# Kernel optimization log

Measured on AMD Instinct MI355X. Metric: run time of the kernel, lower is better.

The kernel has to match this reference:

```python
import jax, jax.numpy as jnp
import numpy as np

B, F, D = 1024, 39, 16
HIDDEN = [128, 128, 128]


def _cin(x, Ws, bs):
    # x: (B, F0, D) stacked field embeddings
    F0 = x.shape[1]
    h = x  # hidden_nn_layers[-1], shape (B, Fk, D)
    outs = []
    n = len(Ws)
    for i, (W, b) in enumerate(zip(Ws, bs)):
        L = W.shape[-1]
        Fk = h.shape[1]
        Wr = W.reshape(F0, Fk, L)  # conv1d kernel [1, F0*Fk, L] -> (F0, Fk, L)
        # per-embedding-dim field outer product: (B, F0, Fk, D)
        z = jnp.einsum('bfd,bgd->bfgd', x, h)
        # pointwise conv over D + bias + relu -> (B, L, D)
        cur = jax.nn.relu(jnp.einsum('bfgd,fgl->bld', z, Wr) + b[None, :, None])
        if i != n - 1:
            h = cur[:, : L // 2]          # next_hidden
            direct = cur[:, L // 2 :]     # direct_connect
        else:
            direct = cur
        outs.append(direct)
    # concat over field axis, sum over embedding dim -> (B, sum_direct)
    return jnp.concatenate(outs, axis=1).sum(-1)


def setup_inputs() -> dict:
    key = jax.random.key(0)
    ks = jax.random.split(key, 8)
    x = jax.random.normal(ks[0], (B, F, D), dtype=jnp.float32)
    field_nums = [F]
    Ws, bs = [], []
    for i, L in enumerate(HIDDEN):
        fan_in = field_nums[0] * field_nums[-1]
        lim = np.sqrt(6.0 / fan_in)  # he_uniform
        Ws.append(jax.random.uniform(ks[1 + i], (fan_in, L), jnp.float32, -lim, lim))
        bs.append(jnp.zeros((L,), jnp.float32))
        field_nums.append(L // 2)
    return {"x": x, "W0": Ws[0], "W1": Ws[1], "W2": Ws[2],
            "b0": bs[0], "b1": bs[1], "b2": bs[2]}


def reference(x, W0, W1, W2, b0, b1, b2):
    return _cin(x, [W0, W1, W2], [b0, b1, b2])
```

## Files before the change

kernel.cpp:

```cpp
#include <hip/hip_runtime.h>


#define NF     39
#define LCH    128
#define NLAYER 3
#define NFT    (NLAYER * NF)
#define BPB    2
#define SL     (BPB * 16)
#define MT     (SL / 16)

typedef __bf16        bf16x8 __attribute__((ext_vector_type(8)));
typedef unsigned int  uint4v __attribute__((ext_vector_type(4)));
typedef float         f32x4  __attribute__((ext_vector_type(4)));

__device__ __forceinline__ unsigned short f2bf_rne(float f) {
    unsigned u = __float_as_uint(f);
    u += 0x7fffu + ((u >> 16) & 1u);
    return (unsigned short)(u >> 16);
}

__global__ void cin_prep(const float* __restrict__ W0,
                         const float* __restrict__ W1,
                         const float* __restrict__ W2,
                         unsigned short* __restrict__ wt)
{
    const int t = blockIdx.x * blockDim.x + threadIdx.x;
    if (t >= NFT * 1024) return;
    const int n  = t & 127;
    const int q  = (t >> 7) & 3;
    const int ks = (t >> 9) & 1;
    const int tl = t >> 10;
    const int l  = tl / NF;
    const int f  = tl - l * NF;
    const float* W = (l == 0) ? W0 : (l == 1) ? W1 : W2;

    unsigned short v[8];
    #pragma unroll
    for (int j = 0; j < 8; ++j) {
        const int g = ks * 32 + q * 8 + j;
        float w = 0.0f;
        if (l == 0) { if (g < NF) w = W[(f * NF + g) * LCH + n]; }
        else        { w = W[(f * 64 + g) * LCH + n]; }
        v[j] = f2bf_rne(w);
    }
    uint4v pv;
    #pragma unroll
    for (int i = 0; i < 4; ++i)
        pv[i] = (unsigned)v[2 * i] | ((unsigned)v[2 * i + 1] << 16);
    ((uint4v*)wt)[t] = pv;
}

__global__ __launch_bounds__(512, 4) void cin_mfma(
    const float* __restrict__ x,
    const unsigned short* __restrict__ wt,
    const float* __restrict__ b0p,
    const float* __restrict__ b1p,
    const float* __restrict__ b2p,
    float* __restrict__ out)
{
    __shared__ __align__(16) unsigned short hfrag[8 * SL * 8];
    __shared__ float xf32[NF * SL];
    __shared__ float biasl[NLAYER * LCH];

    const int tid  = threadIdx.x;
    const int lane = tid & 63;
    const int w    = tid >> 6;
    const int q    = lane >> 4;
    const int c    = lane & 15;
    const int nc   = w * 16 + c;
    const int bb   = blockIdx.x * BPB;

    {
        f32x4 z4 = {0.f, 0.f, 0.f, 0.f};
        if (tid < (8 * SL * 8) / 8) ((f32x4*)hfrag)[tid] = z4;
    }
    for (int t = tid; t < NLAYER * LCH; t += 512)
        biasl[t] = (t < 128) ? b0p[t] : (t < 256) ? b1p[t - 128] : b2p[t - 256];
    __syncthreads();

    for (int i = tid; i < BPB * NF * 16; i += 512) {
        const float v = x[bb * (NF * 16) + i];
        const int lb = i / (NF * 16);
        const int r  = i - lb * (NF * 16);
        const int f  = r >> 4;
        const int d  = r & 15;
        const int sl = lb * 16 + d;
        xf32[f * SL + sl] = v;
        hfrag[((f >> 3) * SL + sl) * 8 + (f & 7)] = f2bf_rne(v);
    }

    const unsigned short* wq = wt + (q * 128 + nc) * 8;

    bf16x8 c0 = *(const bf16x8*)(wq);
    bf16x8 c1 = *(const bf16x8*)(wq + 4096);
    bf16x8 m0 = *(const bf16x8*)(wq + 8192);
    bf16x8 m1 = *(const bf16x8*)(wq + 8192 + 4096);
    bf16x8 n0 = *(const bf16x8*)(wq + 16384);
    bf16x8 n1 = *(const bf16x8*)(wq + 16384 + 4096);

    __syncthreads();

    #pragma unroll 1
    for (int l = 0; l < NLAYER; ++l) {
        bf16x8 a[2][MT];
        #pragma unroll
        for (int ks = 0; ks < 2; ++ks)
            #pragma unroll
            for (int mt = 0; mt < MT; ++mt)
                a[ks][mt] = *(const bf16x8*)&hfrag[((ks * 4 + q) * SL + mt * 16 + c) * 8];

        f32x4 cur[MT];
        #pragma unroll
        for (int mt = 0; mt < MT; ++mt) cur[mt] = f32x4{0.f, 0.f, 0.f, 0.f};
        const f32x4 z = {0.f, 0.f, 0.f, 0.f};

        #pragma unroll 3
        for (int f = 0; f < NF; ++f) {
            const bf16x8 bv0 = c0;
            const bf16x8 bv1 = c1;

            #pragma unroll
            for (int mt = 0; mt < MT; ++mt) {
                f32x4 sv = __builtin_amdgcn_mfma_f32_16x16x32_bf16(a[0][mt], bv0, z,  0, 0, 0);
                sv       = __builtin_amdgcn_mfma_f32_16x16x32_bf16(a[1][mt], bv1, sv, 0, 0, 0);
                const f32x4 xr = *(const f32x4*)&xf32[f * SL + mt * 16 + q * 4];
                #pragma unroll
                for (int r = 0; r < 4; ++r)
                    cur[mt][r] = fmaf(xr[r], sv[r], cur[mt][r]);
            }

            c0 = m0; c1 = m1;
            m0 = n0; m1 = n1;
            int pf = l * NF + f + 3; if (pf > NFT - 1) pf = NFT - 1;
            const unsigned short* p = wq + (size_t)pf * 8192;
            n0 = *(const bf16x8*)p;
            n1 = *(const bf16x8*)(p + 4096);
        }

        const float bias = biasl[l * LCH + nc];
        float v[MT][4];
        #pragma unroll
        for (int mt = 0; mt < MT; ++mt)
            #pragma unroll
            for (int r = 0; r < 4; ++r)
                v[mt][r] = fmaxf(cur[mt][r] + bias, 0.f);

        if (l < 2 && w < 4) {
            #pragma unroll
            for (int mt = 0; mt < MT; ++mt)
                #pragma unroll
                for (int r = 0; r < 4; ++r)
                    hfrag[((nc >> 3) * SL + mt * 16 + q * 4 + r) * 8 + (nc & 7)] =
                        f2bf_rne(v[mt][r]);
        } else {
            const int outcol = (l == 0) ? nc - 64 : (l == 1) ? nc : 128 + nc;
            #pragma unroll
            for (int mt = 0; mt < MT; ++mt) {
                float sacc = v[mt][0] + v[mt][1] + v[mt][2] + v[mt][3];
                sacc += __shfl_xor(sacc, 16, 64);
                sacc += __shfl_xor(sacc, 32, 64);
                if (lane < 16) out[(bb + mt) * 256 + outcol] = sacc;
            }
        }
        if (l < 2) __syncthreads();
    }
}

extern "C" void kernel_launch(void* const* d_in, const int* in_sizes, int n_in,
                              void* d_out, int out_size, void* d_ws, size_t ws_size,
                              hipStream_t stream) {
    const float* x  = (const float*)d_in[0];
    const float* W0 = (const float*)d_in[1];
    const float* W1 = (const float*)d_in[2];
    const float* W2 = (const float*)d_in[3];
    const float* b0 = (const float*)d_in[4];
    const float* b1 = (const float*)d_in[5];
    const float* b2 = (const float*)d_in[6];
    float* out = (float*)d_out;
    unsigned short* wt = (unsigned short*)d_ws;

    const int prep_threads = NFT * 1024;
    cin_prep<<<(prep_threads + 255) / 256, 256, 0, stream>>>(W0, W1, W2, wt);
    cin_mfma<<<1024 / BPB, 512, 0, stream>>>(x, wt, b0, b1, b2, out);
}
```

Baseline: 107.5 us.

## Stage weight tiles in LDS via async double-buffered loads and share across waves

The change doubles the batch rows per block and doubles threads to 1024, with two wave groups along M. Each wave group shares the same weight tiles. Weights are no longer streamed from global memory into registers per wave; they are copied into a double-buffered LDS staging area with global_load_lds, three fields per phase. This halves redundant global weight traffic per batch element and overlaps the next phase's load with the current MFMAs. In exchange it adds a block-wide barrier every three fields and uses about 96KB of LDS, which limits occupancy.

```diff
diff --git a/kernel.cpp b/kernel.cpp
--- a/kernel.cpp
+++ b/kernel.cpp
@@ -1,13 +1,16 @@
 #include <hip/hip_runtime.h>
 
 
-#define NF     39
-#define LCH    128
-#define NLAYER 3
-#define NFT    (NLAYER * NF)
-#define BPB    2
-#define SL     (BPB * 16)
-#define MT     (SL / 16)
+#define NF      39
+#define LCH     128
+#define NLAYER  3
+#define NFT     (NLAYER * NF)
+#define BPB     4
+#define SL      (BPB * 16)
+#define NTHR    1024
+#define TILE_SH 8192
+#define PH_T    3
+#define BUF_SH  (PH_T * TILE_SH)
 
 typedef __bf16        bf16x8 __attribute__((ext_vector_type(8)));
 typedef unsigned int  uint4v __attribute__((ext_vector_type(4)));
@@ -50,7 +53,7 @@
     ((uint4v*)wt)[t] = pv;
 }
 
-__global__ __launch_bounds__(512, 4) void cin_mfma(
+__global__ __launch_bounds__(NTHR, 4) void cin_mfma(
     const float* __restrict__ x,
     const unsigned short* __restrict__ wt,
     const float* __restrict__ b0p,
@@ -58,6 +61,7 @@
     const float* __restrict__ b2p,
     float* __restrict__ out)
 {
+    __shared__ __align__(16) unsigned short Bbuf[2 * BUF_SH];
     __shared__ __align__(16) unsigned short hfrag[8 * SL * 8];
     __shared__ float xf32[NF * SL];
     __shared__ float biasl[NLAYER * LCH];
@@ -65,20 +69,22 @@
     const int tid  = threadIdx.x;
     const int lane = tid & 63;
     const int w    = tid >> 6;
+    const int wn   = w & 7;
+    const int wm   = w >> 3;
     const int q    = lane >> 4;
     const int c    = lane & 15;
-    const int nc   = w * 16 + c;
+    const int nc   = wn * 16 + c;
     const int bb   = blockIdx.x * BPB;
 
-    {
+    if (tid < 512) {
         f32x4 z4 = {0.f, 0.f, 0.f, 0.f};
-        if (tid < (8 * SL * 8) / 8) ((f32x4*)hfrag)[tid] = z4;
-    }
-    for (int t = tid; t < NLAYER * LCH; t += 512)
-        biasl[t] = (t < 128) ? b0p[t] : (t < 256) ? b1p[t - 128] : b2p[t - 256];
+        ((f32x4*)hfrag)[tid] = z4;
+    }
+    if (tid < NLAYER * LCH)
+        biasl[tid] = (tid < 128) ? b0p[tid] : (tid < 256) ? b1p[tid - 128] : b2p[tid - 256];
     __syncthreads();
 
-    for (int i = tid; i < BPB * NF * 16; i += 512) {
+    for (int i = tid; i < BPB * NF * 16; i += NTHR) {
         const float v = x[bb * (NF * 16) + i];
         const int lb = i / (NF * 16);
         const int r  = i - lb * (NF * 16);
@@ -89,77 +95,103 @@
         hfrag[((f >> 3) * SL + sl) * 8 + (f & 7)] = f2bf_rne(v);
     }
 
-    const unsigned short* wq = wt + (q * 128 + nc) * 8;
-
-    bf16x8 c0 = *(const bf16x8*)(wq);
-    bf16x8 c1 = *(const bf16x8*)(wq + 4096);
-    bf16x8 m0 = *(const bf16x8*)(wq + 8192);
-    bf16x8 m1 = *(const bf16x8*)(wq + 8192 + 4096);
-    bf16x8 n0 = *(const bf16x8*)(wq + 16384);
-    bf16x8 n1 = *(const bf16x8*)(wq + 16384 + 4096);
-
+    {
+        const unsigned short* src = wt + w * 512 + lane * 8;
+        unsigned short* dst = Bbuf + w * 512;
+        #pragma unroll
+        for (int k = 0; k < PH_T; ++k)
+            __builtin_amdgcn_global_load_lds((const void*)(src + k * TILE_SH),
+                                             (void*)(dst + k * TILE_SH), 16, 0, 0);
+    }
     __syncthreads();
+
+    const unsigned short* bq = Bbuf + (q * 128 + nc) * 8;
+
+    int cb = 0;
+    int tl = 0;
 
     #pragma unroll 1
     for (int l = 0; l < NLAYER; ++l) {
-        bf16x8 a[2][MT];
+        bf16x8 a[2][2];
         #pragma unroll
         for (int ks = 0; ks < 2; ++ks)
             #pragma unroll
-            for (int mt = 0; mt < MT; ++mt)
-                a[ks][mt] = *(const bf16x8*)&hfrag[((ks * 4 + q) * SL + mt * 16 + c) * 8];
-
-        f32x4 cur[MT];
+            for (int mtl = 0; mtl < 2; ++mtl)
+                a[ks][mtl] = *(const bf16x8*)
+                    &hfrag[((ks * 4 + q) * SL + (wm * 2 + mtl) * 16 + c) * 8];
+
+        f32x4 cur0 = {0.f, 0.f, 0.f, 0.f};
+        f32x4 cur1 = {0.f, 0.f, 0.f, 0.f};
+        const f32x4 z = {0.f, 0.f, 0.f, 0.f};
+
+        #pragma unroll 1
+        for (int ph = 0; ph < NF / PH_T; ++ph) {
+            const int nb = tl + PH_T;
+            if (nb < NFT) {
+                const unsigned short* src = wt + (size_t)nb * TILE_SH + w * 512 + lane * 8;
+                unsigned short* dst = &Bbuf[(cb ^ 1) * BUF_SH + w * 512];
+                #pragma unroll
+                for (int k = 0; k < PH_T; ++k)
+                    __builtin_amdgcn_global_load_lds((const void*)(src + k * TILE_SH),
+                                                     (void*)(dst + k * TILE_SH), 16, 0, 0);
+            }
+
+            const unsigned short* rb = bq + cb * BUF_SH;
+            const bf16x8 B00 = *(const bf16x8*)(rb);
+            const bf16x8 B01 = *(const bf16x8*)(rb + 4096);
+            const bf16x8 B10 = *(const bf16x8*)(rb + TILE_SH);
+            const bf16x8 B11 = *(const bf16x8*)(rb + TILE_SH + 4096);
+            const bf16x8 B20 = *(const bf16x8*)(rb + 2 * TILE_SH);
+            const bf16x8 B21 = *(const bf16x8*)(rb + 2 * TILE_SH + 4096);
+
+            const int f0 = ph * PH_T;
+            #define CIN_ITER(BV0, BV1, FI)                                              \
+            {                                                                           \
+                f32x4 sv0 = __builtin_amdgcn_mfma_f32_16x16x32_bf16(a[0][0], BV0, z, 0, 0, 0); \
+                sv0 = __builtin_amdgcn_mfma_f32_16x16x32_bf16(a[1][0], BV1, sv0, 0, 0, 0);     \
+                f32x4 sv1 = __builtin_amdgcn_mfma_f32_16x16x32_bf16(a[0][1], BV0, z, 0, 0, 0); \
+                sv1 = __builtin_amdgcn_mfma_f32_16x16x32_bf16(a[1][1], BV1, sv1, 0, 0, 0);     \
+                const f32x4 xr0 = *(const f32x4*)&xf32[(FI) * SL + (wm * 2 + 0) * 16 + q * 4]; \
+                const f32x4 xr1 = *(const f32x4*)&xf32[(FI) * SL + (wm * 2 + 1) * 16 + q * 4]; \
+                _Pragma("unroll")                                                       \
+                for (int r = 0; r < 4; ++r) {                                           \
+                    cur0[r] = fmaf(xr0[r], sv0[r], cur0[r]);                            \
+                    cur1[r] = fmaf(xr1[r], sv1[r], cur1[r]);                            \
+                }                                                                       \
+            }
+            CIN_ITER(B00, B01, f0 + 0)
+            CIN_ITER(B10, B11, f0 + 1)
+            CIN_ITER(B20, B21, f0 + 2)
+            #undef CIN_ITER
+
+            __syncthreads();
+            cb ^= 1;
+            tl += PH_T;
+        }
+
+        const float bias = biasl[l * LCH + nc];
+        float v[2][4];
         #pragma unroll
-        for (int mt = 0; mt < MT; ++mt) cur[mt] = f32x4{0.f, 0.f, 0.f, 0.f};
-        const f32x4 z = {0.f, 0.f, 0.f, 0.f};
-
-        #pragma unroll 3
-        for (int f = 0; f < NF; ++f) {
-            const bf16x8 bv0 = c0;
-            const bf16x8 bv1 = c1;
-
+        for (int r = 0; r < 4; ++r) {
+            v[0][r] = fmaxf(cur0[r] + bias, 0.f);
+            v[1][r] = fmaxf(cur1[r] + bias, 0.f);
+        }
+
+        if (l < 2 && wn < 4) {
             #pragma unroll
-            for (int mt = 0; mt < MT; ++mt) {
-                f32x4 sv = __builtin_amdgcn_mfma_f32_16x16x32_bf16(a[0][mt], bv0, z,  0, 0, 0);
-                sv       = __builtin_amdgcn_mfma_f32_16x16x32_bf16(a[1][mt], bv1, sv, 0, 0, 0);
-                const f32x4 xr = *(const f32x4*)&xf32[f * SL + mt * 16 + q * 4];
+            for (int mtl = 0; mtl < 2; ++mtl)
                 #pragma unroll
                 for (int r = 0; r < 4; ++r)
-                    cur[mt][r] = fmaf(xr[r], sv[r], cur[mt][r]);
-            }
-
-            c0 = m0; c1 = m1;
-            m0 = n0; m1 = n1;
-            int pf = l * NF + f + 3; if (pf > NFT - 1) pf = NFT - 1;
-            const unsigned short* p = wq + (size_t)pf * 8192;
-            n0 = *(const bf16x8*)p;
-            n1 = *(const bf16x8*)(p + 4096);
-        }
-
-        const float bias = biasl[l * LCH + nc];
-        float v[MT][4];
-        #pragma unroll
-        for (int mt = 0; mt < MT; ++mt)
-            #pragma unroll
-            for (int r = 0; r < 4; ++r)
-                v[mt][r] = fmaxf(cur[mt][r] + bias, 0.f);
-
-        if (l < 2 && w < 4) {
-            #pragma unroll
-            for (int mt = 0; mt < MT; ++mt)
-                #pragma unroll
-                for (int r = 0; r < 4; ++r)
-                    hfrag[((nc >> 3) * SL + mt * 16 + q * 4 + r) * 8 + (nc & 7)] =
-                        f2bf_rne(v[mt][r]);
+                    hfrag[((nc >> 3) * SL + (wm * 2 + mtl) * 16 + q * 4 + r) * 8 + (nc & 7)] =
+                        f2bf_rne(v[mtl][r]);
         } else {
             const int outcol = (l == 0) ? nc - 64 : (l == 1) ? nc : 128 + nc;
             #pragma unroll
-            for (int mt = 0; mt < MT; ++mt) {
-                float sacc = v[mt][0] + v[mt][1] + v[mt][2] + v[mt][3];
+            for (int mtl = 0; mtl < 2; ++mtl) {
+                float sacc = v[mtl][0] + v[mtl][1] + v[mtl][2] + v[mtl][3];
                 sacc += __shfl_xor(sacc, 16, 64);
                 sacc += __shfl_xor(sacc, 32, 64);
-                if (lane < 16) out[(bb + mt) * 256 + outcol] = sacc;
+                if (lane < 16) out[(bb + wm * 2 + mtl) * 256 + outcol] = sacc;
             }
         }
         if (l < 2) __syncthreads();
@@ -181,5 +213,5 @@
 
     const int prep_threads = NFT * 1024;
     cin_prep<<<(prep_threads + 255) / 256, 256, 0, stream>>>(W0, W1, W2, wt);
-    cin_mfma<<<1024 / BPB, 512, 0, stream>>>(x, wt, b0, b1, b2, out);
-}
+    cin_mfma<<<1024 / BPB, NTHR, 0, stream>>>(x, wt, b0, b1, b2, out);
+}
```

After: 103.0 us. -4.2%, faster.
